# Optimization experiments

Measured on AMD Instinct MI355X. Metric: run time of the kernel, lower is better.

The kernel has to match this reference:

```python
import jax, jax.numpy as jnp
import numpy as np

B, S, D, H = 4, 1024, 1024, 16
DK = D // H
EPS = 1e-6


def setup_inputs() -> dict:
    key = jax.random.key(0)
    ks = jax.random.split(key, 12)
    s = 1.0 / np.sqrt(D)
    inp = {
        "query": jax.random.normal(ks[0], (B, S, D), jnp.float32),
        "key": jax.random.normal(ks[1], (B, S, D), jnp.float32),
        "value": jax.random.normal(ks[2], (B, S, D), jnp.float32),
        "Wq": jax.random.normal(ks[3], (D, D), jnp.float32) * s,
        "bq": jnp.zeros((D,), jnp.float32),
        "Wk": jax.random.normal(ks[4], (D, D), jnp.float32) * s,
        "bk": jnp.zeros((D,), jnp.float32),
        "Wv": jax.random.normal(ks[5], (D, D), jnp.float32) * s,
        "bv": jnp.zeros((D,), jnp.float32),
        "Wo": jax.random.normal(ks[6], (D, D), jnp.float32) * s,
        "bo": jnp.zeros((D,), jnp.float32),
        "gamma": jnp.ones((D,), jnp.float32),
        "beta": jnp.zeros((D,), jnp.float32),
    }
    return inp


def reference(query, key, value, Wq, bq, Wk, bk, Wv, bv, Wo, bo, gamma, beta):
    residual = query
    # QKV projections, split into heads: [B,S,D] -> [B,H,S,DK]
    q = (query @ Wq + bq).reshape(B, S, H, DK).transpose(0, 2, 1, 3)
    k = (key @ Wk + bk).reshape(B, S, H, DK).transpose(0, 2, 1, 3)
    v = (value @ Wv + bv).reshape(B, S, H, DK).transpose(0, 2, 1, 3)
    # scaled dot-product attention (dropout is identity in eval mode)
    scores = jnp.einsum("bhqd,bhkd->bhqk", q, k) / jnp.sqrt(jnp.float32(DK))
    attn = jax.nn.softmax(scores, axis=-1)  # [B,H,S,S]
    x = jnp.einsum("bhqk,bhkd->bhqd", attn, v)
    x = x.transpose(0, 2, 1, 3).reshape(B, S, D)
    # residual + LayerNorm(eps=1e-6)
    x = x + residual
    mu = jnp.mean(x, axis=-1, keepdims=True)
    var = jnp.mean(jnp.square(x - mu), axis=-1, keepdims=True)
    x = (x - mu) * jax.lax.rsqrt(var + EPS) * gamma + beta
    out = x @ Wo + bo
    return (out, attn)
```

## Files before the change

### kernel.cpp

```cpp
#include <hip/hip_runtime.h>

typedef unsigned short u16;
typedef __attribute__((ext_vector_type(8))) short bf16x8;
typedef __attribute__((ext_vector_type(4))) float f32x4;

struct __align__(8) us4 { u16 x, y, z, w; };

#define B_  4
#define S_  1024
#define D_  1024
#define H_  16
#define DK_ 64

__device__ __forceinline__ u16 f2bf(float x) {
    union { float f; unsigned int u; } c; c.f = x;
    unsigned int r = (c.u + 0x7FFFu + ((c.u >> 16) & 1u)) >> 16;
    return (u16)r;
}

__device__ __forceinline__ u16 f2bf_trunc(float x) {
    union { float f; unsigned int u; } c; c.f = x;
    return (u16)(c.u >> 16);
}

__device__ __forceinline__ float bf2f(u16 x) {
    union { unsigned int u; float f; } c; c.u = ((unsigned int)x) << 16;
    return c.f;
}

__device__ __forceinline__ void gload_lds16(const void* g, void* l) {
    __builtin_amdgcn_global_load_lds(
        (const __attribute__((address_space(1))) unsigned int*)g,
        (__attribute__((address_space(3))) unsigned int*)l, 16, 0, 0);
}

__device__ __forceinline__ void nt_store4(f32x4 v, float* p) {
    __builtin_nontemporal_store(v, (f32x4*)p);
}

__global__ __launch_bounds__(256) void cvt_all(const float* __restrict__ q, const float* __restrict__ k,
                                               const float* __restrict__ v,
                                               const float* __restrict__ w0, const float* __restrict__ w1,
                                               const float* __restrict__ w2, const float* __restrict__ w3,
                                               u16* __restrict__ xq, u16* __restrict__ xk, u16* __restrict__ xv,
                                               u16* __restrict__ t0, u16* __restrict__ t1,
                                               u16* __restrict__ t2, u16* __restrict__ t3) {
    __shared__ float t[64][65];
    int bid = blockIdx.x;
    int tid = threadIdx.x;
    if (bid < 12288) {
        int which = bid >> 12;
        int xb = bid & 4095;
        const float* src = (which == 0) ? q : (which == 1) ? k : v;
        u16* dst        = (which == 0) ? xq : (which == 1) ? xk : xv;
        int idx = (xb * 256 + tid) * 4;
        f32x4 f = *(const f32x4*)(src + idx);
        us4 o; o.x = f2bf(f[0]); o.y = f2bf(f[1]); o.z = f2bf(f[2]); o.w = f2bf(f[3]);
        *(us4*)(dst + idx) = o;
    } else {
        int rem = bid - 12288;
        int z = rem >> 8;
        int r2 = rem & 255;
        int kb = r2 >> 4, nb = r2 & 15;
        const float* W = (z == 0) ? w0 : (z == 1) ? w1 : (z == 2) ? w2 : w3;
        u16* T        = (z == 0) ? t0 : (z == 1) ? t1 : (z == 2) ? t2 : t3;
        int k0 = kb * 64, n0 = nb * 64;
        int r4 = tid >> 6, c = tid & 63;
#pragma unroll
        for (int i = 0; i < 16; i++) {
            int r = i * 4 + r4;
            t[r][c] = W[(size_t)(k0 + r) * 1024 + n0 + c];
        }
        __syncthreads();
#pragma unroll
        for (int i = 0; i < 16; i++) {
            int r = i * 4 + r4;
            T[(size_t)(n0 + r) * 1024 + k0 + c] = f2bf(t[c][r]);
        }
    }
}

template <int BN, int MODE>
__device__ __forceinline__ void gemm_core(const u16* __restrict__ X, const u16* __restrict__ WT,
                                          const float* __restrict__ bias, void* __restrict__ outp,
                                          float scale, int bm, int bn) {
    constexpr int NS = BN / 32;
    extern __shared__ u16 smem[];
    u16* Al = smem;
    u16* Bl = smem + 128 * 64;
    int tid = threadIdx.x, l = tid & 63, w = tid >> 6;
    int lr = l & 15, lq = l >> 4;
    int wm = (w >> 1) * 64, wn = (w & 1) * (BN / 2);
    f32x4 acc[4][NS] = {};
    for (int kk = 0; kk < 1024; kk += 64) {
        __syncthreads();
#pragma unroll
        for (int i = 0; i < 4; i++) {
            int flat = tid * 16 + i * 4096;
            int row = flat >> 7, kb = flat & 127;
            int kbs = kb ^ ((row & 7) << 4);
            gload_lds16((const char*)X + ((size_t)(bm * 128 + row) * 2048 + (size_t)kk * 2 + kbs),
                        (char*)Al + flat);
        }
#pragma unroll
        for (int i = 0; i < BN / 32; i++) {
            int flat = tid * 16 + i * 4096;
            int row = flat >> 7, kb = flat & 127;
            int kbs = kb ^ ((row & 7) << 4);
            gload_lds16((const char*)WT + ((size_t)(bn * BN + row) * 2048 + (size_t)kk * 2 + kbs),
                        (char*)Bl + flat);
        }
        asm volatile("s_waitcnt vmcnt(0)" ::: "memory");
        __syncthreads();
#pragma unroll
        for (int kkk = 0; kkk < 2; kkk++) {
            bf16x8 af[4], bfr[NS];
            int colb = kkk * 64 + lq * 16;
#pragma unroll
            for (int ms = 0; ms < 4; ms++) {
                int row = wm + ms * 16 + lr;
                af[ms] = *(const bf16x8*)((const char*)Al + row * 128 + (colb ^ ((row & 7) << 4)));
            }
#pragma unroll
            for (int ns = 0; ns < NS; ns++) {
                int row = wn + ns * 16 + lr;
                bfr[ns] = *(const bf16x8*)((const char*)Bl + row * 128 + (colb ^ ((row & 7) << 4)));
            }
#pragma unroll
            for (int ms = 0; ms < 4; ms++)
#pragma unroll
                for (int ns = 0; ns < NS; ns++) {
                    if (MODE == 1)
                        acc[ms][ns] = __builtin_amdgcn_mfma_f32_16x16x32_bf16(af[ms], bfr[ns], acc[ms][ns], 0, 0, 0);
                    else
                        acc[ms][ns] = __builtin_amdgcn_mfma_f32_16x16x32_bf16(bfr[ns], af[ms], acc[ms][ns], 0, 0, 0);
                }
        }
    }
    if (MODE == 1) {
#pragma unroll
        for (int ns = 0; ns < NS; ns++) {
            int n = bn * BN + wn + ns * 16 + lr;
            float bv_ = bias[n];
            int h = n >> 6, dk = n & 63;
#pragma unroll
            for (int ms = 0; ms < 4; ms++) {
                int mbase = bm * 128 + wm + ms * 16 + lq * 4;
                u16* o = (u16*)outp;
                int b = mbase >> 10, s0 = mbase & 1023;
                us4 pk;
                pk.x = f2bf(acc[ms][ns][0] + bv_);
                pk.y = f2bf(acc[ms][ns][1] + bv_);
                pk.z = f2bf(acc[ms][ns][2] + bv_);
                pk.w = f2bf(acc[ms][ns][3] + bv_);
                *(us4*)(o + ((size_t)(b * H_ + h) * 64 + dk) * 1024 + s0) = pk;
            }
        }
    } else {
#pragma unroll
        for (int ns = 0; ns < NS; ns++) {
            int n0 = bn * BN + wn + ns * 16 + lq * 4;
            f32x4 bv4 = *(const f32x4*)(bias + n0);
#pragma unroll
            for (int ms = 0; ms < 4; ms++) {
                int m = bm * 128 + wm + ms * 16 + lr;
                if (MODE == 0) {
                    u16* o = (u16*)outp;
                    int h = n0 >> 6, dk = n0 & 63;
                    int b = m >> 10, s = m & 1023;
                    us4 pk;
                    pk.x = f2bf((acc[ms][ns][0] + bv4[0]) * scale);
                    pk.y = f2bf((acc[ms][ns][1] + bv4[1]) * scale);
                    pk.z = f2bf((acc[ms][ns][2] + bv4[2]) * scale);
                    pk.w = f2bf((acc[ms][ns][3] + bv4[3]) * scale);
                    *(us4*)(o + ((size_t)(b * H_ + h) * 1024 + s) * 64 + dk) = pk;
                } else {
                    float* o = (float*)outp;
                    f32x4 o4 = acc[ms][ns] + bv4;
                    *(f32x4*)(o + (size_t)m * 1024 + n0) = o4;
                }
            }
        }
    }
}

__global__ __launch_bounds__(256, 3) void gemm_qkv(const u16* __restrict__ Xq, const u16* __restrict__ Xk,
                                                   const u16* __restrict__ Xv,
                                                   const u16* __restrict__ Wq, const u16* __restrict__ Wk,
                                                   const u16* __restrict__ Wv,
                                                   const float* __restrict__ bq, const float* __restrict__ bk,
                                                   const float* __restrict__ bv,
                                                   u16* __restrict__ Qh, u16* __restrict__ Kh,
                                                   u16* __restrict__ VT) {
    int z = blockIdx.z;
    const u16* X = (z == 0) ? Xq : (z == 1) ? Xk : Xv;
    const u16* W = (z == 0) ? Wq : (z == 1) ? Wk : Wv;
    const float* bia = (z == 0) ? bq : (z == 1) ? bk : bv;
    if (z == 2)
        gemm_core<128, 1>(X, W, bia, (void*)VT, 1.0f, blockIdx.x, blockIdx.y);
    else if (z == 0)
        gemm_core<128, 0>(X, W, bia, (void*)Qh, 0.125f, blockIdx.x, blockIdx.y);
    else
        gemm_core<128, 0>(X, W, bia, (void*)Kh, 1.0f, blockIdx.x, blockIdx.y);
}

__global__ __launch_bounds__(256, 3) void gemm_out(const u16* __restrict__ X, const u16* __restrict__ WT,
                                                   const float* __restrict__ bias, float* __restrict__ outp) {
    gemm_core<64, 2>(X, WT, bias, outp, 1.0f, blockIdx.x, blockIdx.y);
}

__global__ __launch_bounds__(256, 4) void attn_fused(const u16* __restrict__ Qh, const u16* __restrict__ Kh,
                                                     const u16* __restrict__ VT,
                                                     float* __restrict__ attn_out, float* __restrict__ x_out) {
    __shared__ u16 P_lds[16 * 1024];
    __shared__ float reds[4][16];
    int tid = threadIdx.x, l = tid & 63, w = tid >> 6;
    int lr = l & 15, lq = l >> 4;

    for (int t = blockIdx.x; t < 4096; t += 1024) {
        int xcd = t & 7;
        int rest = t >> 3;
        int bh = ((rest & 7) << 3) | xcd;
        int q0 = (rest >> 3) * 16;
        const u16* qp = Qh + (size_t)bh * 65536;
        const u16* kp = Kh + (size_t)bh * 65536;
        const u16* vp = VT + (size_t)bh * 65536;

        bf16x8 bq0 = *(const bf16x8*)(qp + (q0 + lr) * 64 + lq * 8);
        bf16x8 bq1 = *(const bf16x8*)(qp + (q0 + lr) * 64 + 32 + lq * 8);

        float s = 0.f;
#pragma unroll 4
        for (int n = 0; n < 16; n++) {
            int kb = w * 256 + n * 16;
            bf16x8 a0 = *(const bf16x8*)(kp + (size_t)(kb + lr) * 64 + lq * 8);
            bf16x8 a1 = *(const bf16x8*)(kp + (size_t)(kb + lr) * 64 + 32 + lq * 8);
            f32x4 a = {};
            a = __builtin_amdgcn_mfma_f32_16x16x32_bf16(a0, bq0, a, 0, 0, 0);
            a = __builtin_amdgcn_mfma_f32_16x16x32_bf16(a1, bq1, a, 0, 0, 0);
            f32x4 e;
            e[0] = __expf(a[0]); e[1] = __expf(a[1]);
            e[2] = __expf(a[2]); e[3] = __expf(a[3]);
            s += e[0] + e[1] + e[2] + e[3];
            int col = w * 256 + n * 16 + lq * 4;
            us4 pk;
            pk.x = f2bf_trunc(e[0]); pk.y = f2bf_trunc(e[1]);
            pk.z = f2bf_trunc(e[2]); pk.w = f2bf_trunc(e[3]);
            *(us4*)&P_lds[lr * 1024 + (col ^ ((lr & 7) << 3))] = pk;
        }
        s += __shfl_xor(s, 16);
        s += __shfl_xor(s, 32);
        if (l < 16) reds[w][lr] = s;
        __syncthreads();

        size_t abase = (size_t)bh * 1048576 + (size_t)q0 * 1024;
#pragma unroll
        for (int i = 0; i < 16; i++) {
            float inv_i = 1.0f / (reds[0][i] + reds[1][i] + reds[2][i] + reds[3][i]);
            us4 pk4 = *(const us4*)&P_lds[i * 1024 + ((tid * 4) ^ ((i & 7) << 3))];
            f32x4 o;
            o[0] = bf2f(pk4.x) * inv_i;
            o[1] = bf2f(pk4.y) * inv_i;
            o[2] = bf2f(pk4.z) * inv_i;
            o[3] = bf2f(pk4.w) * inv_i;
            nt_store4(o, attn_out + abase + (size_t)i * 1024 + tid * 4);
        }

        f32x4 pv[8] = {};
#pragma unroll
        for (int kk = 0; kk < 32; kk++) {
            bf16x8 ap = *(const bf16x8*)&P_lds[lr * 1024 + ((kk * 32 + lq * 8) ^ ((lr & 7) << 3))];
            bf16x8 bv = *(const bf16x8*)(vp + (size_t)(w * 16 + lr) * 1024 + kk * 32 + lq * 8);
            pv[kk & 7] = __builtin_amdgcn_mfma_f32_16x16x32_bf16(ap, bv, pv[kk & 7], 0, 0, 0);
        }
#pragma unroll
        for (int c = 4; c >= 1; c >>= 1)
#pragma unroll
            for (int i = 0; i < c; i++) pv[i] += pv[i + c];

        int b = bh >> 4, h = bh & 15;
#pragma unroll
        for (int r = 0; r < 4; r++) {
            int row = lq * 4 + r;
            float inv = 1.0f / (reds[0][row] + reds[1][row] + reds[2][row] + reds[3][row]);
            __builtin_nontemporal_store(pv[0][r] * inv,
                x_out + ((size_t)(b * 1024 + q0 + row)) * 1024 + h * 64 + w * 16 + lr);
        }
        __syncthreads();
    }
}

__global__ __launch_bounds__(256) void ln_kernel(const float* __restrict__ x, const float* __restrict__ resid,
                                                 const float* __restrict__ gamma, const float* __restrict__ beta,
                                                 u16* __restrict__ out) {
    __shared__ float as_[4], as2_[4];
    int row = blockIdx.x, tid = threadIdx.x;
    int l = tid & 63, w = tid >> 6;
    size_t base = (size_t)row * 1024 + tid * 4;
    f32x4 v = *(const f32x4*)(x + base);
    f32x4 rz = *(const f32x4*)(resid + base);
    v += rz;
    float s = v[0] + v[1] + v[2] + v[3];
    float s2 = v[0] * v[0] + v[1] * v[1] + v[2] * v[2] + v[3] * v[3];
#pragma unroll
    for (int off = 1; off < 64; off <<= 1) {
        s += __shfl_xor(s, off);
        s2 += __shfl_xor(s2, off);
    }
    if (l == 0) { as_[w] = s; as2_[w] = s2; }
    __syncthreads();
    s = as_[0] + as_[1] + as_[2] + as_[3];
    s2 = as2_[0] + as2_[1] + as2_[2] + as2_[3];
    float mean = s * (1.f / 1024.f);
    float var = s2 * (1.f / 1024.f) - mean * mean;
    float rs = rsqrtf(var + 1e-6f);
    f32x4 g = *(const f32x4*)(gamma + tid * 4);
    f32x4 bt = *(const f32x4*)(beta + tid * 4);
    us4 o;
    o.x = f2bf((v[0] - mean) * rs * g[0] + bt[0]);
    o.y = f2bf((v[1] - mean) * rs * g[1] + bt[1]);
    o.z = f2bf((v[2] - mean) * rs * g[2] + bt[2]);
    o.w = f2bf((v[3] - mean) * rs * g[3] + bt[3]);
    *(us4*)(out + base) = o;
}

extern "C" void kernel_launch(void* const* d_in, const int* in_sizes, int n_in,
                              void* d_out, int out_size, void* d_ws, size_t ws_size,
                              hipStream_t stream) {
    const float* query = (const float*)d_in[0];
    const float* key   = (const float*)d_in[1];
    const float* value = (const float*)d_in[2];
    const float* Wq    = (const float*)d_in[3];
    const float* bq    = (const float*)d_in[4];
    const float* Wk    = (const float*)d_in[5];
    const float* bk    = (const float*)d_in[6];
    const float* Wv    = (const float*)d_in[7];
    const float* bv    = (const float*)d_in[8];
    const float* Wo    = (const float*)d_in[9];
    const float* bo    = (const float*)d_in[10];
    const float* gamma = (const float*)d_in[11];
    const float* beta  = (const float*)d_in[12];

    char* ws = (char*)d_ws;
    u16* XQ  = (u16*)(ws + 0);
    u16* XK  = (u16*)(ws + 8388608);
    u16* XV  = (u16*)(ws + 16777216);
    u16* WQT = (u16*)(ws + 25165824);
    u16* WKT = (u16*)(ws + 27262976);
    u16* WVT = (u16*)(ws + 29360128);
    u16* WOT = (u16*)(ws + 31457280);
    u16* Qh  = (u16*)(ws + 33554432);
    u16* Kh  = (u16*)(ws + 41943040);
    u16* VT  = (u16*)(ws + 50331648);
    float* PV = (float*)(ws + 0);
    u16* LN  = (u16*)(ws + 16777216);

    float* outp = (float*)d_out;
    float* attn = outp + 4194304;

    cvt_all<<<dim3(13312), 256, 0, stream>>>(query, key, value, Wq, Wk, Wv, Wo,
                                             XQ, XK, XV, WQT, WKT, WVT, WOT);
    gemm_qkv<<<dim3(32, 8, 3), 256, 32768, stream>>>(XQ, XK, XV, WQT, WKT, WVT, bq, bk, bv, Qh, Kh, VT);
    attn_fused<<<dim3(1024), 256, 0, stream>>>(Qh, Kh, VT, attn, PV);
    ln_kernel<<<4096, 256, 0, stream>>>(PV, query, gamma, beta, LN);
    gemm_out<<<dim3(32, 16), 256, 24576, stream>>>(LN, WOT, bo, outp);
}
```

Measured before the change: 250.9 us.

## Split fused attention into softmax kernel and separate tiled PV GEMM

The fused attention kernel is split in two. attn_qk computes QK^T, the exponentials and the normalized attention matrix and writes it to the output. A new pv_gemm kernel then reads that fp32 attention matrix back, converts it to bf16 in LDS and multiplies it by V with 128x64 tiles. This is meant to remove the PV work from the fused kernel, which read V straight from global memory with little reuse and a long serial MFMA chain. The cost is an extra read of the 64M-element fp32 attention matrix from HBM plus one more kernel launch.

Measured after the change: 254.5 us. Within noise of the previous version (+1.4%).

```diff
diff --git a/kernel.cpp b/kernel.cpp
--- a/kernel.cpp
+++ b/kernel.cpp
@@ -209,84 +209,128 @@
     gemm_core<64, 2>(X, WT, bias, outp, 1.0f, blockIdx.x, blockIdx.y);
 }
 
-__global__ __launch_bounds__(256, 4) void attn_fused(const u16* __restrict__ Qh, const u16* __restrict__ Kh,
-                                                     const u16* __restrict__ VT,
-                                                     float* __restrict__ attn_out, float* __restrict__ x_out) {
+__global__ void attn_qk(const u16* __restrict__ Qh, const u16* __restrict__ Kh,
+                        float* __restrict__ attn_out) {
     __shared__ u16 P_lds[16 * 1024];
     __shared__ float reds[4][16];
     int tid = threadIdx.x, l = tid & 63, w = tid >> 6;
     int lr = l & 15, lq = l >> 4;
-
-    for (int t = blockIdx.x; t < 4096; t += 1024) {
-        int xcd = t & 7;
-        int rest = t >> 3;
-        int bh = ((rest & 7) << 3) | xcd;
-        int q0 = (rest >> 3) * 16;
-        const u16* qp = Qh + (size_t)bh * 65536;
-        const u16* kp = Kh + (size_t)bh * 65536;
-        const u16* vp = VT + (size_t)bh * 65536;
-
-        bf16x8 bq0 = *(const bf16x8*)(qp + (q0 + lr) * 64 + lq * 8);
-        bf16x8 bq1 = *(const bf16x8*)(qp + (q0 + lr) * 64 + 32 + lq * 8);
-
-        float s = 0.f;
+    int wg = blockIdx.x;
+    int xcd = wg & 7;
+    int rest = wg >> 3;
+    int q0 = (rest & 63) * 16;
+    int bh = ((rest >> 6) << 3) | xcd;
+    const u16* qp = Qh + (size_t)bh * 65536;
+    const u16* kp = Kh + (size_t)bh * 65536;
+
+    bf16x8 bq0 = *(const bf16x8*)(qp + (q0 + lr) * 64 + lq * 8);
+    bf16x8 bq1 = *(const bf16x8*)(qp + (q0 + lr) * 64 + 32 + lq * 8);
+
+    float s = 0.f;
 #pragma unroll 4
-        for (int n = 0; n < 16; n++) {
-            int kb = w * 256 + n * 16;
-            bf16x8 a0 = *(const bf16x8*)(kp + (size_t)(kb + lr) * 64 + lq * 8);
-            bf16x8 a1 = *(const bf16x8*)(kp + (size_t)(kb + lr) * 64 + 32 + lq * 8);
-            f32x4 a = {};
-            a = __builtin_amdgcn_mfma_f32_16x16x32_bf16(a0, bq0, a, 0, 0, 0);
-            a = __builtin_amdgcn_mfma_f32_16x16x32_bf16(a1, bq1, a, 0, 0, 0);
-            f32x4 e;
-            e[0] = __expf(a[0]); e[1] = __expf(a[1]);
-            e[2] = __expf(a[2]); e[3] = __expf(a[3]);
-            s += e[0] + e[1] + e[2] + e[3];
-            int col = w * 256 + n * 16 + lq * 4;
+    for (int n = 0; n < 16; n++) {
+        int kb = w * 256 + n * 16;
+        bf16x8 a0 = *(const bf16x8*)(kp + (size_t)(kb + lr) * 64 + lq * 8);
+        bf16x8 a1 = *(const bf16x8*)(kp + (size_t)(kb + lr) * 64 + 32 + lq * 8);
+        f32x4 a = {};
+        a = __builtin_amdgcn_mfma_f32_16x16x32_bf16(a0, bq0, a, 0, 0, 0);
+        a = __builtin_amdgcn_mfma_f32_16x16x32_bf16(a1, bq1, a, 0, 0, 0);
+        f32x4 e;
+        e[0] = __expf(a[0]); e[1] = __expf(a[1]);
+        e[2] = __expf(a[2]); e[3] = __expf(a[3]);
+        s += e[0] + e[1] + e[2] + e[3];
+        int col = w * 256 + n * 16 + lq * 4;
+        us4 pk;
+        pk.x = f2bf_trunc(e[0]); pk.y = f2bf_trunc(e[1]);
+        pk.z = f2bf_trunc(e[2]); pk.w = f2bf_trunc(e[3]);
+        *(us4*)&P_lds[lr * 1024 + (col ^ ((lr & 7) << 3))] = pk;
+    }
+    s += __shfl_xor(s, 16);
+    s += __shfl_xor(s, 32);
+    if (l < 16) reds[w][lr] = s;
+    __syncthreads();
+
+    size_t abase = (size_t)bh * 1048576 + (size_t)q0 * 1024;
+#pragma unroll
+    for (int i = 0; i < 16; i++) {
+        float inv_i = 1.0f / (reds[0][i] + reds[1][i] + reds[2][i] + reds[3][i]);
+        us4 pk4 = *(const us4*)&P_lds[i * 1024 + ((tid * 4) ^ ((i & 7) << 3))];
+        f32x4 o;
+        o[0] = bf2f(pk4.x) * inv_i;
+        o[1] = bf2f(pk4.y) * inv_i;
+        o[2] = bf2f(pk4.z) * inv_i;
+        o[3] = bf2f(pk4.w) * inv_i;
+        nt_store4(o, attn_out + abase + (size_t)i * 1024 + tid * 4);
+    }
+}
+
+__global__ __launch_bounds__(256, 2) void pv_gemm(const float* __restrict__ attnP,
+                                                  const u16* __restrict__ VT,
+                                                  float* __restrict__ x_out) {
+    __shared__ u16 Pl[128 * 64];
+    __shared__ u16 Vl[64 * 64];
+    int bid = blockIdx.x;
+    int bh = bid >> 3, stile = bid & 7;
+    int b = bh >> 4, h = bh & 15;
+    const float* pp = attnP + (size_t)bh * 1048576 + (size_t)stile * 131072;
+    const u16* vp = VT + (size_t)bh * 65536;
+    int tid = threadIdx.x, l = tid & 63, w = tid >> 6;
+    int lr = l & 15, lq = l >> 4;
+    int wm = (w >> 1) * 64, wn = (w & 1) * 32;
+    int pcol = tid & 15;
+    int prow0 = tid >> 4;
+    f32x4 acc[4][2] = {};
+    for (int kk = 0; kk < 16; kk++) {
+        __syncthreads();
+#pragma unroll
+        for (int i = 0; i < 2; i++) {
+            int flat = tid * 16 + i * 4096;
+            int row = flat >> 7, kb = flat & 127;
+            int kbs = kb ^ ((row & 7) << 4);
+            gload_lds16((const char*)vp + (size_t)row * 2048 + (size_t)kk * 128 + kbs,
+                        (char*)Vl + flat);
+        }
+#pragma unroll
+        for (int j = 0; j < 8; j++) {
+            int row = prow0 + j * 16;
+            f32x4 f = *(const f32x4*)(pp + (size_t)row * 1024 + kk * 64 + pcol * 4);
             us4 pk;
-            pk.x = f2bf_trunc(e[0]); pk.y = f2bf_trunc(e[1]);
-            pk.z = f2bf_trunc(e[2]); pk.w = f2bf_trunc(e[3]);
-            *(us4*)&P_lds[lr * 1024 + (col ^ ((lr & 7) << 3))] = pk;
-        }
-        s += __shfl_xor(s, 16);
-        s += __shfl_xor(s, 32);
-        if (l < 16) reds[w][lr] = s;
+            pk.x = f2bf_trunc(f[0]); pk.y = f2bf_trunc(f[1]);
+            pk.z = f2bf_trunc(f[2]); pk.w = f2bf_trunc(f[3]);
+            int colb = pcol * 8;
+            *(us4*)((char*)Pl + row * 128 + (colb ^ ((row & 7) << 4))) = pk;
+        }
+        asm volatile("s_waitcnt vmcnt(0)" ::: "memory");
         __syncthreads();
-
-        size_t abase = (size_t)bh * 1048576 + (size_t)q0 * 1024;
-#pragma unroll
-        for (int i = 0; i < 16; i++) {
-            float inv_i = 1.0f / (reds[0][i] + reds[1][i] + reds[2][i] + reds[3][i]);
-            us4 pk4 = *(const us4*)&P_lds[i * 1024 + ((tid * 4) ^ ((i & 7) << 3))];
-            f32x4 o;
-            o[0] = bf2f(pk4.x) * inv_i;
-            o[1] = bf2f(pk4.y) * inv_i;
-            o[2] = bf2f(pk4.z) * inv_i;
-            o[3] = bf2f(pk4.w) * inv_i;
-            nt_store4(o, attn_out + abase + (size_t)i * 1024 + tid * 4);
-        }
-
-        f32x4 pv[8] = {};
-#pragma unroll
-        for (int kk = 0; kk < 32; kk++) {
-            bf16x8 ap = *(const bf16x8*)&P_lds[lr * 1024 + ((kk * 32 + lq * 8) ^ ((lr & 7) << 3))];
-            bf16x8 bv = *(const bf16x8*)(vp + (size_t)(w * 16 + lr) * 1024 + kk * 32 + lq * 8);
-            pv[kk & 7] = __builtin_amdgcn_mfma_f32_16x16x32_bf16(ap, bv, pv[kk & 7], 0, 0, 0);
-        }
-#pragma unroll
-        for (int c = 4; c >= 1; c >>= 1)
-#pragma unroll
-            for (int i = 0; i < c; i++) pv[i] += pv[i + c];
-
-        int b = bh >> 4, h = bh & 15;
-#pragma unroll
-        for (int r = 0; r < 4; r++) {
-            int row = lq * 4 + r;
-            float inv = 1.0f / (reds[0][row] + reds[1][row] + reds[2][row] + reds[3][row]);
-            __builtin_nontemporal_store(pv[0][r] * inv,
-                x_out + ((size_t)(b * 1024 + q0 + row)) * 1024 + h * 64 + w * 16 + lr);
-        }
-        __syncthreads();
+#pragma unroll
+        for (int kkk = 0; kkk < 2; kkk++) {
+            int colb = kkk * 64 + lq * 16;
+            bf16x8 af[4], bfr[2];
+#pragma unroll
+            for (int ms = 0; ms < 4; ms++) {
+                int row = wm + ms * 16 + lr;
+                af[ms] = *(const bf16x8*)((const char*)Pl + row * 128 + (colb ^ ((row & 7) << 4)));
+            }
+#pragma unroll
+            for (int ns = 0; ns < 2; ns++) {
+                int row = wn + ns * 16 + lr;
+                bfr[ns] = *(const bf16x8*)((const char*)Vl + row * 128 + (colb ^ ((row & 7) << 4)));
+            }
+#pragma unroll
+            for (int ms = 0; ms < 4; ms++)
+#pragma unroll
+                for (int ns = 0; ns < 2; ns++)
+                    acc[ms][ns] = __builtin_amdgcn_mfma_f32_16x16x32_bf16(bfr[ns], af[ms], acc[ms][ns], 0, 0, 0);
+        }
+    }
+#pragma unroll
+    for (int ns = 0; ns < 2; ns++) {
+        int n0 = wn + ns * 16 + lq * 4;
+#pragma unroll
+        for (int ms = 0; ms < 4; ms++) {
+            int m = stile * 128 + wm + ms * 16 + lr;
+            nt_store4(acc[ms][ns], x_out + ((size_t)(b * 1024 + m)) * 1024 + h * 64 + n0);
+        }
     }
 }
 
@@ -361,7 +405,8 @@
     cvt_all<<<dim3(13312), 256, 0, stream>>>(query, key, value, Wq, Wk, Wv, Wo,
                                              XQ, XK, XV, WQT, WKT, WVT, WOT);
     gemm_qkv<<<dim3(32, 8, 3), 256, 32768, stream>>>(XQ, XK, XV, WQT, WKT, WVT, bq, bk, bv, Qh, Kh, VT);
-    attn_fused<<<dim3(1024), 256, 0, stream>>>(Qh, Kh, VT, attn, PV);
+    attn_qk<<<dim3(4096), 256, 0, stream>>>(Qh, Kh, attn);
+    pv_gemm<<<dim3(512), 256, 0, stream>>>(attn, VT, PV);
     ln_kernel<<<4096, 256, 0, stream>>>(PV, query, gamma, beta, LN);
     gemm_out<<<dim3(32, 16), 256, 24576, stream>>>(LN, WOT, bo, outp);
 }
```
